# Performance work log

Hardware: AMD Instinct MI355X
Metric: run time of the kernel (lower is better)

The kernel has to match this reference:

```python
import jax, jax.numpy as jnp
import numpy as np

NEG = -9e9  # large negative used by the original torch code for masking


def setup_inputs() -> dict:
    key = jax.random.key(0)
    k1, k2, k3, k4 = jax.random.split(key, 4)
    B, N, L, D = 64, 128, 64, 768
    return {
        "text_embeddings": jax.random.normal(k1, (B, N, D), dtype=jnp.float32),
        "image_embeddings": jax.random.normal(k2, (B, L, D), dtype=jnp.float32),
        "text_mask": jax.random.randint(k3, (B, N), 0, 2, dtype=jnp.int32),
        "image_mask": jax.random.randint(k4, (B, L), 0, 2, dtype=jnp.int32),
    }


def _grounding(text_emb, image_emb, text_mask, image_mask):
    # Vectorized version of the B x B python loop in score_grounding.
    tm = text_mask.astype(text_emb.dtype)   # [B, N]
    im = image_mask.astype(text_emb.dtype)  # [B, L]
    # pairwise mask: mask[i, j, n, l] = text_mask[i, n] * image_mask[j, l]
    mask = tm[:, None, :, None] * im[None, :, None, :]            # [B, B, N, L]
    att = jnp.einsum('ind,jld->ijnl', text_emb, image_emb) * mask  # [B, B, N, L]
    att = jnp.where(att * mask != 0, att, NEG)
    # softmax over image spans (last dim), masked
    aw_first = jax.nn.softmax(att, axis=-1) * mask
    score1 = (aw_first * att).sum(-1).mean(-1)                     # [B, B]
    # softmax over text spans (dim 2 == the N axis), masked (transpose trick in torch)
    aw_second = jax.nn.softmax(att, axis=2) * mask
    score2 = (aw_second * att).sum(-1).mean(-1)                    # [B, B]
    sent_scores = score1 + score2                                  # [B, B]
    B = text_emb.shape[0]
    idx = jnp.arange(B)
    token_scores = att[idx, idx]                                   # diagonal pairs, [B, N, L]
    return sent_scores, token_scores


def reference(text_embeddings, image_embeddings, text_mask, image_mask):
    B = text_embeddings.shape[0]
    S, token_scores = _grounding(text_embeddings, image_embeddings, text_mask, image_mask)
    # text_emb_i2s = softmax(att_weights) @ image_emb
    text_emb_i2s = jnp.einsum('bnl,bld->bnd', jax.nn.softmax(token_scores, axis=-1), image_embeddings)
    # loss = -(sum diag logsoftmax(S, dim=1) + sum diag logsoftmax(S.T, dim=1)) / n
    ls1 = jnp.diagonal(jax.nn.log_softmax(S, axis=1))
    ls2 = jnp.diagonal(jax.nn.log_softmax(S.T, axis=1))
    loss = -(jnp.sum(ls1) + jnp.sum(ls2)) / B
    return loss, text_emb_i2s
```

## Files before the change

kernel.cpp:

```cpp
#include <hip/hip_runtime.h>
#include <math.h>

#define BSZ 64
#define NN  128
#define LL  64
#define DD  768
#define NEGV (-9e9f)

#define TQ (BSZ * NN * DD / 4)
#define IQ (BSZ * LL * DD / 4)

typedef _Float16 f16x8 __attribute__((ext_vector_type(8)));
typedef __attribute__((ext_vector_type(4))) float f32x4;

__device__ __forceinline__ void gl_lds16(const void* g, void* l) {
    __builtin_amdgcn_global_load_lds(
        (const __attribute__((address_space(1))) void*)g,
        (__attribute__((address_space(3))) void*)l, 16, 0, 0);
}

__global__ __launch_bounds__(256) void k_prep(
    const float4* __restrict__ t4, const float4* __restrict__ g4,
    ushort4* __restrict__ A, ushort4* __restrict__ B)
{
    int id = blockIdx.x * 256 + threadIdx.x;
    const float4* src; ushort4* dst; int idx;
    if (id < TQ) { src = t4; dst = A; idx = id; }
    else         { src = g4; dst = B; idx = id - TQ; }
    float4 x = src[idx];
    _Float16 h0 = (_Float16)x.x, h1 = (_Float16)x.y;
    _Float16 h2 = (_Float16)x.z, h3 = (_Float16)x.w;
    ushort4 o;
    o.x = __builtin_bit_cast(unsigned short, h0);
    o.y = __builtin_bit_cast(unsigned short, h1);
    o.z = __builtin_bit_cast(unsigned short, h2);
    o.w = __builtin_bit_cast(unsigned short, h3);
    dst[idx] = o;
}

__device__ __forceinline__ void stage_chunk(
    const unsigned short* __restrict__ pa, const unsigned short* __restrict__ pb,
    int k0, char* buf, int wave, int lane)
{
    int rsub = lane >> 3;
    int k8s  = lane & 7;
#pragma unroll
    for (int c = 0; c < 4; c++) {
        int r  = c * 32 + wave * 8 + rsub;
        int k8 = k8s ^ (r & 7);
        gl_lds16(pa + (size_t)r * DD + k0 + k8 * 8, buf + c * 4096 + wave * 1024);
        gl_lds16(pb + (size_t)r * DD + k0 + k8 * 8, buf + 16384 + c * 4096 + wave * 1024);
    }
}

__global__ __launch_bounds__(256, 2) void k_scores(
    const unsigned short* __restrict__ A, const unsigned short* __restrict__ B,
    const int* __restrict__ tmask, const int* __restrict__ imask,
    float* __restrict__ S, float* __restrict__ W)
{
    union SmemU {
        char  stage[2][32768];
        float Cs[NN][129];
    };
    __shared__ SmemU u;
    __shared__ float tmi[NN];
    __shared__ float imj[NN];
    __shared__ float rowred[256];
    __shared__ float colred[NN];
    __shared__ float rowm[256], rowsm[256];
    __shared__ float colm[256], colp1[256], colp2[256];

    const int bid = blockIdx.x;
    const int grp = bid >> 4, idx = bid & 15;
    const int i  = (grp >> 3) * 4 + (idx >> 2);
    const int jj = (grp & 7) * 4 + (idx & 3);
    const int j0 = jj * 2;

    const int tid  = threadIdx.x;
    const int wave = tid >> 6;
    const int lane = tid & 63;
    const int quad = lane >> 4;
    const int l15  = lane & 15;
    const int rh   = wave & 1;
    const int ch   = wave >> 1;

    if (tid < NN) {
        tmi[tid] = tmask[i * NN + tid] ? 1.f : 0.f;
        imj[tid] = imask[j0 * LL + tid] ? 1.f : 0.f;
    }

    const unsigned short* pa = A + (size_t)i * NN * DD;
    const unsigned short* pb = B + (size_t)j0 * LL * DD;

    f32x4 acc[4][4];
    const f32x4 zf = {0.f, 0.f, 0.f, 0.f};
#pragma unroll
    for (int tr = 0; tr < 4; tr++)
#pragma unroll
        for (int tc = 0; tc < 4; tc++) acc[tr][tc] = zf;

    stage_chunk(pa, pb, 0, u.stage[0], wave, lane);
    __syncthreads();

    for (int c = 0; c < 12; c++) {
        if (c + 1 < 12)
            stage_chunk(pa, pb, (c + 1) << 6, u.stage[(c + 1) & 1], wave, lane);
        const char* Ab = u.stage[c & 1];
        const char* Bb = Ab + 16384;
#pragma unroll
        for (int s = 0; s < 2; s++) {
            int k8q = s * 4 + quad;
            int sw  = k8q ^ (l15 & 7);
            f16x8 af[4], bfr[4];
#pragma unroll
            for (int t = 0; t < 4; t++) {
                int row = rh * 64 + t * 16 + l15;
                af[t]  = *(const f16x8*)(Ab + ((row << 3) + sw) * 16);
                int col = ch * 64 + t * 16 + l15;
                bfr[t] = *(const f16x8*)(Bb + ((col << 3) + sw) * 16);
            }
#pragma unroll
            for (int tr = 0; tr < 4; tr++)
#pragma unroll
                for (int tc = 0; tc < 4; tc++)
                    acc[tr][tc] = __builtin_amdgcn_mfma_f32_16x16x32_f16(
                        af[tr], bfr[tc], acc[tr][tc], 0, 0, 0);
        }
        __syncthreads();
    }

#pragma unroll
    for (int tr = 0; tr < 4; tr++) {
        int rb = rh * 64 + tr * 16 + quad * 4;
#pragma unroll
        for (int tc = 0; tc < 4; tc++) {
            int col = ch * 64 + tc * 16 + l15;
            float im = imj[col];
#pragma unroll
            for (int rr = 0; rr < 4; rr++) {
                int row = rb + rr;
                float v = acc[tr][tc][rr];
                bool keep = (tmi[row] != 0.f) && (im != 0.f) && (v != 0.f);
                u.Cs[row][col] = keep ? v : NEGV;
            }
        }
    }
    __syncthreads();

    {
        int jh = tid >> 7, n = tid & 127;
        const float* Crow = &u.Cs[n][jh * 64];
        float m = -INFINITY;
        for (int l = 0; l < LL; l++) m = fmaxf(m, Crow[l]);
        float ssum = 0.f, ws = 0.f;
        for (int l = 0; l < LL; l++) {
            float v = Crow[l];
            float e = __expf(v - m);
            ssum += e;
            ws += imj[jh * 64 + l] * e * v;
        }
        rowm[tid] = m;
        rowsm[tid] = ssum;
        rowred[tid] = tmi[n] * (ws / ssum);
    }
    __syncthreads();

    {
        int c  = tid & 127;
        int n0 = (tid >> 7) * 64;
        float m = -INFINITY;
        for (int n = n0; n < n0 + 64; n++) m = fmaxf(m, u.Cs[n][c]);
        colm[tid] = m;
        __syncthreads();
        m = fmaxf(colm[tid], colm[tid ^ 128]);
        float ssum = 0.f, ws = 0.f;
        for (int n = n0; n < n0 + 64; n++) {
            float v = u.Cs[n][c];
            float e = __expf(v - m);
            ssum += e;
            ws += tmi[n] * e * v;
        }
        colp1[tid] = ssum;
        colp2[tid] = ws;
    }
    __syncthreads();
    if (tid < NN) {
        float ssum = colp1[tid] + colp1[tid + 128];
        float ws   = colp2[tid] + colp2[tid + 128];
        colred[tid] = imj[tid] * (ws / ssum);
    }

    if (jj == (i >> 1) && tid < NN) {
        int jh = i & 1;
        int n = tid;
        float m   = rowm[jh * 128 + n];
        float inv = 1.f / rowsm[jh * 128 + n];
        const float* Crow = &u.Cs[n][jh * 64];
        float* Wb = W + (size_t)i * LL * NN;
        for (int l = 0; l < LL; l++)
            Wb[(size_t)l * NN + n] = __expf(Crow[l] - m) * inv;
    }
    __syncthreads();

    if (tid < NN) {
        int jh = tid >> 6, t = tid & 63;
        float p = rowred[jh * 128 + t] + rowred[jh * 128 + 64 + t] + colred[jh * 64 + t];
#pragma unroll
        for (int off = 32; off; off >>= 1) p += __shfl_down(p, off);
        if (t == 0) S[i * BSZ + j0 + jh] = p / (float)NN;
    }
}

__global__ __launch_bounds__(256) void k_i2s(
    const float* __restrict__ W, const float* __restrict__ img,
    const float* __restrict__ S, float* __restrict__ out)
{
    __shared__ float Ws[LL][64];
    const int b  = blockIdx.x;
    const int ng = blockIdx.z * 64;
    const int d  = blockIdx.y * 256 + threadIdx.x;
    const float* Wb = W + (size_t)b * LL * NN;

    {
#pragma unroll
        for (int rep = 0; rep < 4; rep++) {
            int fidx = (rep * 256 + threadIdx.x) * 4;
            int l = fidx >> 6, noff = fidx & 63;
            float4 w = *(const float4*)(Wb + (size_t)l * NN + ng + noff);
            *(float4*)(&Ws[l][noff]) = w;
        }
    }
    __syncthreads();

    const float* ib = img + (size_t)b * LL * DD;
    float* ob = out + 1 + (size_t)b * NN * DD + (size_t)ng * DD;

    float acc[64];
#pragma unroll
    for (int q = 0; q < 64; q++) acc[q] = 0.f;
    for (int l = 0; l < LL; l++) {
        float g = ib[(size_t)l * DD + d];
#pragma unroll
        for (int q = 0; q < 64; q++)
            acc[q] = fmaf(Ws[l][q], g, acc[q]);
    }
#pragma unroll
    for (int q = 0; q < 64; q++)
        ob[(size_t)q * DD + d] = acc[q];

    if (blockIdx.x == 0 && blockIdx.y == 0 && blockIdx.z == 0 && threadIdx.x < 64) {
        const int t = threadIdx.x;
        float diag = S[t * BSZ + t];
        float m1 = -INFINITY, m2 = -INFINITY;
        for (int jj = 0; jj < BSZ; jj++) {
            m1 = fmaxf(m1, S[t * BSZ + jj]);
            m2 = fmaxf(m2, S[jj * BSZ + t]);
        }
        float s1 = 0.f, s2 = 0.f;
        for (int jj = 0; jj < BSZ; jj++) {
            s1 += __expf(S[t * BSZ + jj] - m1);
            s2 += __expf(S[jj * BSZ + t] - m2);
        }
        float p = 2.f * diag - (m1 + logf(s1)) - (m2 + logf(s2));
#pragma unroll
        for (int off = 32; off; off >>= 1) p += __shfl_down(p, off);
        if (t == 0) out[0] = -p / (float)BSZ;
    }
}

extern "C" void kernel_launch(void* const* d_in, const int* in_sizes, int n_in,
                              void* d_out, int out_size, void* d_ws, size_t ws_size,
                              hipStream_t stream)
{
    (void)in_sizes; (void)n_in; (void)out_size; (void)ws_size;
    const float* text = (const float*)d_in[0];
    const float* img  = (const float*)d_in[1];
    const int*   tm   = (const int*)d_in[2];
    const int*   im   = (const int*)d_in[3];
    float* out = (float*)d_out;

    char* ws = (char*)d_ws;
    unsigned short* A = (unsigned short*)(ws);
    unsigned short* B = (unsigned short*)(ws + 12582912);
    float* S = (float*)(ws + 18874368);
    float* W = (float*)(ws + 18890752);

    k_prep<<<(TQ + IQ) / 256, 256, 0, stream>>>(
        (const float4*)text, (const float4*)img, (ushort4*)A, (ushort4*)B);

    k_scores<<<BSZ * (BSZ / 2), 256, 0, stream>>>(A, B, tm, im, S, W);

    dim3 g2(BSZ, 3, 2);
    k_i2s<<<g2, 256, 0, stream>>>(W, img, S, out);
}
```

Baseline: 198.0 us.

## Compute i2s output with fp16 MFMA using fp16 weights and transposed image

The diagonal softmax weights are now stored in fp16 in an [n][l] layout. A new transpose kernel writes the fp16 image embeddings as [d][l] into the reused A buffer. The i2s product then runs on 16x16x32 fp16 MFMA instructions instead of scalar fp32 FMAs. This cuts the fp32 weight traffic and ALU work, at the cost of an extra kernel launch and lower precision for the weights and image operand in the output.

After: 182.3 us. 7.9% less time.

```diff
diff --git a/kernel.cpp b/kernel.cpp
--- a/kernel.cpp
+++ b/kernel.cpp
@@ -56,7 +56,7 @@
 __global__ __launch_bounds__(256, 2) void k_scores(
     const unsigned short* __restrict__ A, const unsigned short* __restrict__ B,
     const int* __restrict__ tmask, const int* __restrict__ imask,
-    float* __restrict__ S, float* __restrict__ W)
+    float* __restrict__ S, unsigned short* __restrict__ Wh)
 {
     union SmemU {
         char  stage[2][32768];
@@ -196,9 +196,11 @@
         float m   = rowm[jh * 128 + n];
         float inv = 1.f / rowsm[jh * 128 + n];
         const float* Crow = &u.Cs[n][jh * 64];
-        float* Wb = W + (size_t)i * LL * NN;
-        for (int l = 0; l < LL; l++)
-            Wb[(size_t)l * NN + n] = __expf(Crow[l] - m) * inv;
+        unsigned short* Wb = Wh + (size_t)i * NN * LL + (size_t)n * LL;
+        for (int l = 0; l < LL; l++) {
+            _Float16 h = (_Float16)(__expf(Crow[l] - m) * inv);
+            Wb[l] = __builtin_bit_cast(unsigned short, h);
+        }
     }
     __syncthreads();
 
@@ -211,45 +213,90 @@
     }
 }
 
+__global__ __launch_bounds__(256) void k_tr(
+    const unsigned short* __restrict__ B, unsigned short* __restrict__ BT)
+{
+    __shared__ unsigned short Ls[64][136];
+    const int b  = blockIdx.x;
+    const int dc = blockIdx.y;
+    const unsigned short* Bb = B + (size_t)b * LL * DD + dc * 128;
+#pragma unroll
+    for (int rep = 0; rep < 4; rep++) {
+        int idx = rep * 256 + threadIdx.x;
+        int l = idx >> 4, d8 = (idx & 15) * 8;
+        ushort4 v0 = *(const ushort4*)(Bb + (size_t)l * DD + d8);
+        ushort4 v1 = *(const ushort4*)(Bb + (size_t)l * DD + d8 + 4);
+        *(ushort4*)(&Ls[l][d8])     = v0;
+        *(ushort4*)(&Ls[l][d8 + 4]) = v1;
+    }
+    __syncthreads();
+    unsigned short* BTb = BT + (size_t)b * DD * LL + (size_t)dc * 128 * LL;
+#pragma unroll
+    for (int rep = 0; rep < 4; rep++) {
+        int idx = rep * 256 + threadIdx.x;
+        int d = idx >> 3, l0 = (idx & 7) * 8;
+        ushort4 lo, hi;
+        lo.x = Ls[l0 + 0][d]; lo.y = Ls[l0 + 1][d];
+        lo.z = Ls[l0 + 2][d]; lo.w = Ls[l0 + 3][d];
+        hi.x = Ls[l0 + 4][d]; hi.y = Ls[l0 + 5][d];
+        hi.z = Ls[l0 + 6][d]; hi.w = Ls[l0 + 7][d];
+        *(ushort4*)(BTb + (size_t)d * LL + l0)     = lo;
+        *(ushort4*)(BTb + (size_t)d * LL + l0 + 4) = hi;
+    }
+}
+
 __global__ __launch_bounds__(256) void k_i2s(
-    const float* __restrict__ W, const float* __restrict__ img,
+    const unsigned short* __restrict__ Wh, const unsigned short* __restrict__ BT,
     const float* __restrict__ S, float* __restrict__ out)
 {
-    __shared__ float Ws[LL][64];
-    const int b  = blockIdx.x;
-    const int ng = blockIdx.z * 64;
-    const int d  = blockIdx.y * 256 + threadIdx.x;
-    const float* Wb = W + (size_t)b * LL * NN;
-
-    {
-#pragma unroll
-        for (int rep = 0; rep < 4; rep++) {
-            int fidx = (rep * 256 + threadIdx.x) * 4;
-            int l = fidx >> 6, noff = fidx & 63;
-            float4 w = *(const float4*)(Wb + (size_t)l * NN + ng + noff);
-            *(float4*)(&Ws[l][noff]) = w;
-        }
-    }
-    __syncthreads();
-
-    const float* ib = img + (size_t)b * LL * DD;
-    float* ob = out + 1 + (size_t)b * NN * DD + (size_t)ng * DD;
-
-    float acc[64];
-#pragma unroll
-    for (int q = 0; q < 64; q++) acc[q] = 0.f;
-    for (int l = 0; l < LL; l++) {
-        float g = ib[(size_t)l * DD + d];
-#pragma unroll
-        for (int q = 0; q < 64; q++)
-            acc[q] = fmaf(Ws[l][q], g, acc[q]);
-    }
-#pragma unroll
-    for (int q = 0; q < 64; q++)
-        ob[(size_t)q * DD + d] = acc[q];
-
-    if (blockIdx.x == 0 && blockIdx.y == 0 && blockIdx.z == 0 && threadIdx.x < 64) {
-        const int t = threadIdx.x;
+    const int b   = blockIdx.x;
+    const int dc  = blockIdx.y;
+    const int tid = threadIdx.x;
+    const int wave = tid >> 6, lane = tid & 63;
+    const int quad = lane >> 4, l15 = lane & 15;
+    const int nb = (wave >> 1) * 64;
+    const int db = dc * 128 + (wave & 1) * 64;
+
+    const unsigned short* Wb = Wh + (size_t)b * NN * LL;
+    const unsigned short* Bb = BT + (size_t)b * DD * LL;
+
+    f32x4 acc[4][4];
+    const f32x4 zf = {0.f, 0.f, 0.f, 0.f};
+#pragma unroll
+    for (int tn = 0; tn < 4; tn++)
+#pragma unroll
+        for (int td = 0; td < 4; td++) acc[tn][td] = zf;
+
+#pragma unroll
+    for (int s = 0; s < 2; s++) {
+        f16x8 af[4], bf[4];
+#pragma unroll
+        for (int t = 0; t < 4; t++) {
+            af[t] = *(const f16x8*)(Wb + (size_t)(nb + t * 16 + l15) * LL + s * 32 + quad * 8);
+            bf[t] = *(const f16x8*)(Bb + (size_t)(db + t * 16 + l15) * LL + s * 32 + quad * 8);
+        }
+#pragma unroll
+        for (int tn = 0; tn < 4; tn++)
+#pragma unroll
+            for (int td = 0; td < 4; td++)
+                acc[tn][td] = __builtin_amdgcn_mfma_f32_16x16x32_f16(
+                    af[tn], bf[td], acc[tn][td], 0, 0, 0);
+    }
+
+    float* ob = out + 1 + (size_t)b * NN * DD;
+#pragma unroll
+    for (int tn = 0; tn < 4; tn++)
+#pragma unroll
+        for (int td = 0; td < 4; td++)
+#pragma unroll
+            for (int rr = 0; rr < 4; rr++) {
+                int n = nb + tn * 16 + quad * 4 + rr;
+                int d = db + td * 16 + l15;
+                ob[(size_t)n * DD + d] = acc[tn][td][rr];
+            }
+
+    if (blockIdx.x == 0 && blockIdx.y == 0 && tid < 64) {
+        const int t = tid;
         float diag = S[t * BSZ + t];
         float m1 = -INFINITY, m2 = -INFINITY;
         for (int jj = 0; jj < BSZ; jj++) {
@@ -280,16 +327,20 @@
     float* out = (float*)d_out;
 
     char* ws = (char*)d_ws;
-    unsigned short* A = (unsigned short*)(ws);
-    unsigned short* B = (unsigned short*)(ws + 12582912);
-    float* S = (float*)(ws + 18874368);
-    float* W = (float*)(ws + 18890752);
+    unsigned short* A  = (unsigned short*)(ws);
+    unsigned short* B  = (unsigned short*)(ws + 12582912);
+    float*          S  = (float*)(ws + 18874368);
+    unsigned short* Wh = (unsigned short*)(ws + 18890752);
+    unsigned short* BT = A;
 
     k_prep<<<(TQ + IQ) / 256, 256, 0, stream>>>(
         (const float4*)text, (const float4*)img, (ushort4*)A, (ushort4*)B);
 
-    k_scores<<<BSZ * (BSZ / 2), 256, 0, stream>>>(A, B, tm, im, S, W);
-
-    dim3 g2(BSZ, 3, 2);
-    k_i2s<<<g2, 256, 0, stream>>>(W, img, S, out);
-}
+    k_scores<<<BSZ * (BSZ / 2), 256, 0, stream>>>(A, B, tm, im, S, Wh);
+
+    dim3 gt(BSZ, 6);
+    k_tr<<<gt, 256, 0, stream>>>(B, BT);
+
+    dim3 g2(BSZ, 6);
+    k_i2s<<<g2, 256, 0, stream>>>(Wh, BT, S, out);
+}
```
